# Optimization experiments

Hardware: AMD Instinct MI355X
Metric: run time of the kernel (lower is better)

## Reference

```python
import jax, jax.numpy as jnp
import numpy as np

A, B, S, AD, H, NH = 8, 32768, 128, 16, 64, 4
D = H // NH  # attend_dim = 16
MAX_ACTION = 1.0


def setup_inputs() -> dict:
    key = jax.random.key(0)
    ks = jax.random.split(key, 16)
    sc = 0.05
    return {
        'states': jax.random.normal(ks[0], (A, B, S), jnp.float32),
        'actions': jax.random.normal(ks[1], (A, B, AD), jnp.float32),
        'Ws': jax.random.normal(ks[2], (S, H), jnp.float32) * sc,
        'bs': jnp.zeros((H,), jnp.float32),
        'We': jax.random.normal(ks[3], (S + AD, H), jnp.float32) * sc,
        'be': jnp.zeros((H,), jnp.float32),
        'Wk': jax.random.normal(ks[4], (NH, H, D), jnp.float32) * sc,
        'Wsel': jax.random.normal(ks[5], (NH, H, D), jnp.float32) * sc,
        'Wv': jax.random.normal(ks[6], (NH, H, D), jnp.float32) * sc,
        'bv': jnp.zeros((NH, D), jnp.float32),
        'W1': jax.random.normal(ks[7], (2 * H, H), jnp.float32) * sc,
        'b1': jnp.zeros((H,), jnp.float32),
        'W2': jax.random.normal(ks[8], (H, 1), jnp.float32) * sc,
        'b2': jnp.zeros((1,), jnp.float32),
    }


def reference(states, actions, Ws, bs, We, be, Wk, Wsel, Wv, bv, W1, b1, W2, b2):
    # per-agent encoders (shared params, as in the torch module)
    s_enc = jax.nn.relu(jnp.einsum('abs,sh->abh', states, Ws) + bs)          # [A,B,H]
    sa = jnp.concatenate([states, actions / MAX_ACTION], axis=-1)            # [A,B,S+AD]
    sa_enc = jax.nn.relu(jnp.einsum('abi,ih->abh', sa, We) + be)             # [A,B,H]

    # per-head keys / values / selectors (n = head axis)
    keys = jnp.einsum('abh,nhd->nabd', sa_enc, Wk)                           # [NH,A,B,D]
    vals = jax.nn.relu(jnp.einsum('abh,nhd->nabd', sa_enc, Wv) + bv[:, None, None, :])
    sel = jnp.einsum('abh,nhd->nabd', s_enc, Wsel)                           # [NH,A,B,D]

    # exclude-self attention over agents == masked softmax over agent axis j
    logits = jnp.einsum('nibd,njbd->nibj', sel, keys) / jnp.sqrt(jnp.float32(D))
    self_mask = jnp.eye(A, dtype=bool)                                       # [A(i),A(j)]
    logits = jnp.where(self_mask[None, :, None, :], -1e9, logits)
    w = jax.nn.softmax(logits, axis=-1)                                      # [NH,A,B,A]
    other = jnp.einsum('nibj,njbd->nibd', w, vals)                           # [NH,A,B,D]
    other_cat = jnp.transpose(other, (1, 2, 0, 3)).reshape(A, B, NH * D)     # [A,B,H]

    critic_in = jnp.concatenate([sa_enc, other_cat], axis=-1)                # [A,B,2H]
    h = jax.nn.relu(jnp.einsum('abi,ih->abh', critic_in, W1) + b1)
    q = jnp.einsum('abh,ho->abo', h, W2) + b2                                # [A,B,1]
    return q
```

## Files before the change

kernel.cpp:

```cpp
#include <hip/hip_runtime.h>
#include <hip/hip_bf16.h>

#define A_N 8
#define B_N 32768
#define S_N 128
#define AD_N 16

typedef __attribute__((ext_vector_type(8))) short short8;
typedef __attribute__((ext_vector_type(4))) float floatx4;
typedef __attribute__((ext_vector_type(4))) int intx4;

#define MFMA16(a, b, c) __builtin_amdgcn_mfma_f32_16x16x32_bf16(a, b, c, 0, 0, 0)
#define SBAR() __builtin_amdgcn_sched_barrier(0)

__device__ __forceinline__ short f2bf(float f) {
    __hip_bfloat16 h = __float2bfloat16(f);
    return *reinterpret_cast<short*>(&h);
}
__device__ __forceinline__ int pk(float a, float b) {
    __hip_bfloat162 p = __float22bfloat162_rn(make_float2(a, b));
    return *reinterpret_cast<int*>(&p);
}
__device__ __forceinline__ short8 mk8(int a, int b, int c, int d) {
    intx4 v = {a, b, c, d};
    return *reinterpret_cast<short8*>(&v);
}
__device__ __forceinline__ void pk2(short8& r, int i, float a, float b) {
    __hip_bfloat162 p = __float22bfloat162_rn(make_float2(a, b));
    short2 s = *reinterpret_cast<short2*>(&p);
    r[i] = s.x; r[i + 1] = s.y;
}
__device__ __forceinline__ short8 cvt8(float4 x0, float4 x1) {
    short8 r;
    pk2(r, 0, x0.x, x0.y); pk2(r, 2, x0.z, x0.w);
    pk2(r, 4, x1.x, x1.y); pk2(r, 6, x1.z, x1.w);
    return r;
}

__device__ __forceinline__ int chperm(int p) {
    return 32 * (p >> 5) + 16 * ((p & 7) >> 2) + 4 * ((p >> 3) & 3) + (p & 3);
}

#define OFF_Ws   10752
#define OFF_Wk   21504
#define OFF_Wsel 26112
#define OFF_Wv   30720
#define OFF_W1   35328
#define W_TOTAL  44032

__global__ void prep_weights(const float* __restrict__ Ws, const float* __restrict__ bs,
                             const float* __restrict__ We, const float* __restrict__ be,
                             const float* __restrict__ Wk, const float* __restrict__ Wsel,
                             const float* __restrict__ Wv, const float* __restrict__ W1,
                             short* __restrict__ w) {
    int idx = blockIdx.x * 256 + threadIdx.x;
    if (idx >= W_TOTAL) return;
    float v = 0.f;
    if (idx < OFF_Ws) {
        int n = idx / 168, p = idx % 168;
        v = (p < 144) ? We[p * 64 + n] : (p == 144 ? be[n] : 0.f);
    } else if (idx < OFF_Wk) {
        int i = idx - OFF_Ws; int n = i / 168, p = i % 168;
        v = (p < 128) ? Ws[p * 64 + n] : (p == 144 ? bs[n] : 0.f);
    } else if (idx < OFF_Wsel) {
        int i = idx - OFF_Wk; int n = i / 72, p = i % 72;
        if (p < 64) v = Wk[(n >> 4) * 1024 + chperm(p) * 16 + (n & 15)];
    } else if (idx < OFF_Wv) {
        int i = idx - OFF_Wsel; int n = i / 72, p = i % 72;
        if (p < 64) v = Wsel[(n >> 4) * 1024 + chperm(p) * 16 + (n & 15)];
    } else if (idx < OFF_W1) {
        int i = idx - OFF_Wv; int n = i / 72, p = i % 72;
        if (p < 64) v = Wv[(n >> 4) * 1024 + chperm(p) * 16 + (n & 15)];
    } else {
        int i = idx - OFF_W1; int n = i / 136, p = i % 136;
        if (p < 128) v = W1[chperm(p) * 64 + n];
    }
    w[idx] = f2bf(v);
}

#define TILES 8

__global__ __launch_bounds__(512, 2)
void attention_critic_mfma(
    const float* __restrict__ states, const float* __restrict__ actions,
    const float* __restrict__ bv, const float* __restrict__ b1,
    const float* __restrict__ W2, const float* __restrict__ b2,
    const short* __restrict__ wts, float* __restrict__ out)
{
    __shared__ __align__(16) short smem[W_TOTAL];
    const short* lWe   = smem;
    const short* lWs   = smem + OFF_Ws;
    const short* lWk   = smem + OFF_Wk;
    const short* lWsel = smem + OFF_Wsel;
    const short* lWv   = smem + OFF_Wv;
    const short* lW1   = smem + OFF_W1;

    const int tid  = threadIdx.x;
    const int wv   = tid >> 6;
    const int lane = tid & 63;
    const int lq   = lane >> 4;
    const int ln   = lane & 15;

    for (int c = wv; c < 86; c += 8) {
        const unsigned int* g = reinterpret_cast<const unsigned int*>(wts + c * 512) + lane * 4;
        __builtin_amdgcn_global_load_lds(g, reinterpret_cast<unsigned int*>(smem + c * 512), 16, 0, 0);
    }

    float bv4[4], b14[4], w24[4];
    #pragma unroll
    for (int nt = 0; nt < 4; ++nt) {
        bv4[nt] = bv[nt * 16 + ln];
        b14[nt] = b1[nt * 16 + ln];
        w24[nt] = W2[nt * 16 + ln];
    }
    const float b2v = b2[0];

    const int bbase = blockIdx.x * (TILES * 16);
    const int aA  = ln & 7;
    const int blA = ln >> 3;
    const float* srow = states  + ((long)aA * B_N + bbase + wv * 2 + blA) * S_N;
    const float* arow = actions + ((long)aA * B_N + bbase + wv * 2 + blA) * AD_N;

    __syncthreads();

    const floatx4 z  = {0.f, 0.f, 0.f, 0.f};
    const short8  z8 = {0, 0, 0, 0, 0, 0, 0, 0};

    #pragma unroll 1
    for (int t = 0; t < TILES; ++t) {
        const int b0 = bbase + t * 16;

        short8 xf[5];
        #pragma unroll
        for (int s = 0; s < 4; ++s) {
            float4 f0 = *reinterpret_cast<const float4*>(srow + s * 32 + lq * 8);
            float4 f1 = *reinterpret_cast<const float4*>(srow + s * 32 + lq * 8 + 4);
            xf[s] = cvt8(f0, f1);
        }
        {
            short8 xt = z8;
            if (lq < 2) {
                float4 f0 = *reinterpret_cast<const float4*>(arow + lq * 8);
                float4 f1 = *reinterpret_cast<const float4*>(arow + lq * 8 + 4);
                xt = cvt8(f0, f1);
            } else if (lq == 2) {
                xt[0] = (short)0x3F80;
            }
            xf[4] = xt;
        }
        srow += 16 * S_N; arow += 16 * AD_N;

        short8 fE[2];
        {
            floatx4 accE[4] = {z, z, z, z};
            #pragma unroll
            for (int s = 0; s < 5; ++s) {
                const int kk = s * 32 + lq * 8;
                #pragma unroll
                for (int nt = 0; nt < 4; ++nt)
                    accE[nt] = MFMA16(*reinterpret_cast<const short8*>(lWe + (nt * 16 + ln) * 168 + kk), xf[s], accE[nt]);
            }
            int pE[4][2];
            #pragma unroll
            for (int nt = 0; nt < 4; ++nt) {
                pE[nt][0] = pk(fmaxf(accE[nt][0], 0.f), fmaxf(accE[nt][1], 0.f));
                pE[nt][1] = pk(fmaxf(accE[nt][2], 0.f), fmaxf(accE[nt][3], 0.f));
            }
            fE[0] = mk8(pE[0][0], pE[0][1], pE[1][0], pE[1][1]);
            fE[1] = mk8(pE[2][0], pE[2][1], pE[3][0], pE[3][1]);
        }
        SBAR();

        short8 fS[2];
        {
            floatx4 accS[4] = {z, z, z, z};
            #pragma unroll
            for (int s = 0; s < 5; ++s) {
                if (s == 4 && lq != 2) {
                }
                const int kk = s * 32 + lq * 8;
                #pragma unroll
                for (int nt = 0; nt < 4; ++nt)
                    accS[nt] = MFMA16(*reinterpret_cast<const short8*>(lWs + (nt * 16 + ln) * 168 + kk), xf[s], accS[nt]);
            }
            int pS[4][2];
            #pragma unroll
            for (int nt = 0; nt < 4; ++nt) {
                pS[nt][0] = pk(fmaxf(accS[nt][0], 0.f), fmaxf(accS[nt][1], 0.f));
                pS[nt][1] = pk(fmaxf(accS[nt][2], 0.f), fmaxf(accS[nt][3], 0.f));
            }
            fS[0] = mk8(pS[0][0], pS[0][1], pS[1][0], pS[1][1]);
            fS[1] = mk8(pS[2][0], pS[2][1], pS[3][0], pS[3][1]);
        }
        SBAR();

        int kp[4][2], sp[4][2];
        {
            floatx4 accK[4] = {z, z, z, z}, accSl[4] = {z, z, z, z};
            #pragma unroll
            for (int s = 0; s < 2; ++s) {
                const int kk = s * 32 + lq * 8;
                #pragma unroll
                for (int nt = 0; nt < 4; ++nt) {
                    const int rw = (nt * 16 + ln);
                    accK[nt]  = MFMA16(*reinterpret_cast<const short8*>(lWk   + rw * 72 + kk), fE[s], accK[nt]);
                    accSl[nt] = MFMA16(*reinterpret_cast<const short8*>(lWsel + rw * 72 + kk), fS[s], accSl[nt]);
                }
            }
            #pragma unroll
            for (int nt = 0; nt < 4; ++nt) {
                kp[nt][0] = pk(accK[nt][0],  accK[nt][1]);
                kp[nt][1] = pk(accK[nt][2],  accK[nt][3]);
                sp[nt][0] = pk(accSl[nt][0], accSl[nt][1]);
                sp[nt][1] = pk(accSl[nt][2], accSl[nt][3]);
            }
        }
        SBAR();

        int pV[4][2];
        {
            floatx4 accV[4] = {z, z, z, z};
            #pragma unroll
            for (int s = 0; s < 2; ++s) {
                const int kk = s * 32 + lq * 8;
                #pragma unroll
                for (int nt = 0; nt < 4; ++nt)
                    accV[nt] = MFMA16(fE[s], *reinterpret_cast<const short8*>(lWv + (nt * 16 + ln) * 72 + kk), accV[nt]);
            }
            #pragma unroll
            for (int nt = 0; nt < 4; ++nt) {
                pV[nt][0] = pk(fmaxf(accV[nt][0] + bv4[nt], 0.f), fmaxf(accV[nt][1] + bv4[nt], 0.f));
                pV[nt][1] = pk(fmaxf(accV[nt][2] + bv4[nt], 0.f), fmaxf(accV[nt][3] + bv4[nt], 0.f));
            }
        }
        SBAR();

        int pO[4][2];
        {
            const bool sameb = ((lq >> 1) == (ln >> 3));
            #pragma unroll
            for (int nt = 0; nt < 4; ++nt) {
                short8 fa = mk8(kp[nt][0], kp[nt][1], 0, 0);
                short8 fb = mk8(sp[nt][0], sp[nt][1], 0, 0);
                floatx4 L = MFMA16(fa, fb, z);
                float lg[4];
                #pragma unroll
                for (int i = 0; i < 4; ++i) {
                    const bool valid = sameb && (4 * lq + i != ln);
                    lg[i] = valid ? L[i] * 0.25f : -1e9f;
                }
                float m = fmaxf(fmaxf(lg[0], lg[1]), fmaxf(lg[2], lg[3]));
                m = fmaxf(m, __shfl_xor(m, 16, 64));
                m = fmaxf(m, __shfl_xor(m, 32, 64));
                float e0 = __expf(lg[0] - m), e1 = __expf(lg[1] - m);
                float e2 = __expf(lg[2] - m), e3 = __expf(lg[3] - m);
                float ss = e0 + e1 + e2 + e3;
                ss += __shfl_xor(ss, 16, 64);
                ss += __shfl_xor(ss, 32, 64);
                const float inv = 1.f / ss;
                short8 fp = mk8(pk(e0 * inv, e1 * inv), pk(e2 * inv, e3 * inv), 0, 0);
                short8 fv = mk8(pV[nt][0], pV[nt][1], 0, 0);
                floatx4 O = MFMA16(fv, fp, z);
                pO[nt][0] = pk(O[0], O[1]);
                pO[nt][1] = pk(O[2], O[3]);
            }
        }
        SBAR();

        {
            short8 fO[2] = { mk8(pO[0][0], pO[0][1], pO[1][0], pO[1][1]),
                             mk8(pO[2][0], pO[2][1], pO[3][0], pO[3][1]) };
            floatx4 accH[4] = {z, z, z, z};
            #pragma unroll
            for (int s = 0; s < 4; ++s) {
                const int kk = s * 32 + lq * 8;
                const short8 af = (s < 2) ? fE[s] : fO[s - 2];
                #pragma unroll
                for (int nt = 0; nt < 4; ++nt)
                    accH[nt] = MFMA16(af, *reinterpret_cast<const short8*>(lW1 + (nt * 16 + ln) * 136 + kk), accH[nt]);
            }
            float p0 = 0.f, p1 = 0.f, p2 = 0.f, p3 = 0.f;
            #pragma unroll
            for (int nt = 0; nt < 4; ++nt) {
                p0 += fmaxf(accH[nt][0] + b14[nt], 0.f) * w24[nt];
                p1 += fmaxf(accH[nt][1] + b14[nt], 0.f) * w24[nt];
                p2 += fmaxf(accH[nt][2] + b14[nt], 0.f) * w24[nt];
                p3 += fmaxf(accH[nt][3] + b14[nt], 0.f) * w24[nt];
            }
            #pragma unroll
            for (int mk = 1; mk < 16; mk <<= 1) {
                p0 += __shfl_xor(p0, mk, 64);
                p1 += __shfl_xor(p1, mk, 64);
                p2 += __shfl_xor(p2, mk, 64);
                p3 += __shfl_xor(p3, mk, 64);
            }
            if (ln == 0) {
                float pr[4] = {p0, p1, p2, p3};
                #pragma unroll
                for (int i = 0; i < 4; ++i) {
                    const int slot = lq * 4 + i;
                    out[(long)(slot & 7) * B_N + b0 + wv * 2 + (slot >> 3)] = pr[i] + b2v;
                }
            }
        }
        SBAR();
    }
}

extern "C" void kernel_launch(void* const* d_in, const int* in_sizes, int n_in,
                              void* d_out, int out_size, void* d_ws, size_t ws_size,
                              hipStream_t stream) {
    const float* states  = (const float*)d_in[0];
    const float* actions = (const float*)d_in[1];
    const float* Ws      = (const float*)d_in[2];
    const float* bs      = (const float*)d_in[3];
    const float* We      = (const float*)d_in[4];
    const float* be      = (const float*)d_in[5];
    const float* Wk      = (const float*)d_in[6];
    const float* Wsel    = (const float*)d_in[7];
    const float* Wv      = (const float*)d_in[8];
    const float* bv      = (const float*)d_in[9];
    const float* W1      = (const float*)d_in[10];
    const float* b1      = (const float*)d_in[11];
    const float* W2      = (const float*)d_in[12];
    const float* b2      = (const float*)d_in[13];
    short* wts = (short*)d_ws;
    float* out = (float*)d_out;

    prep_weights<<<(W_TOTAL + 255) / 256, 256, 0, stream>>>(Ws, bs, We, be, Wk, Wsel, Wv, W1, wts);
    attention_critic_mfma<<<B_N / (TILES * 16), 512, 0, stream>>>(
        states, actions, bv, b1, W2, b2, wts, out);
}
```

Baseline: 234.3 us.

## Repack LDS weights into MFMA fragment order and raise occupancy with smaller tiles

Reorders the bf16 weight blob so each lane's 8-element MFMA fragment sits contiguously in lane-major order, with no padding. This shrinks LDS from about 88KB to 78KB and gives simple constant-offset ds_read_b128 addresses. The s_enc bias moves out of the packed K=160 slot into a register add, which drops the fifth MFMA step for the Ws projection. TILES goes from 8 to 4, doubling the grid, and launch bounds ask for 4 blocks/CU, which may fail to fit LDS or may force register spilling.

```diff
diff --git a/kernel.cpp b/kernel.cpp
--- a/kernel.cpp
+++ b/kernel.cpp
@@ -41,59 +41,53 @@
     return 32 * (p >> 5) + 16 * ((p & 7) >> 2) + 4 * ((p >> 3) & 3) + (p & 3);
 }
 
-#define OFF_Ws   10752
-#define OFF_Wk   21504
-#define OFF_Wsel 26112
-#define OFF_Wv   30720
-#define OFF_W1   35328
-#define W_TOTAL  44032
-
-__global__ void prep_weights(const float* __restrict__ Ws, const float* __restrict__ bs,
-                             const float* __restrict__ We, const float* __restrict__ be,
+#define OFF_Ws   10240
+#define OFF_Wk   18432
+#define OFF_Wsel 22528
+#define OFF_Wv   26624
+#define OFF_W1   30720
+#define W_TOTAL  38912
+
+__global__ void prep_weights(const float* __restrict__ Ws, const float* __restrict__ We,
+                             const float* __restrict__ be,
                              const float* __restrict__ Wk, const float* __restrict__ Wsel,
                              const float* __restrict__ Wv, const float* __restrict__ W1,
                              short* __restrict__ w) {
     int idx = blockIdx.x * 256 + threadIdx.x;
     if (idx >= W_TOTAL) return;
     float v = 0.f;
-    if (idx < OFF_Ws) {
-        int n = idx / 168, p = idx % 168;
-        v = (p < 144) ? We[p * 64 + n] : (p == 144 ? be[n] : 0.f);
-    } else if (idx < OFF_Wk) {
-        int i = idx - OFF_Ws; int n = i / 168, p = i % 168;
-        v = (p < 128) ? Ws[p * 64 + n] : (p == 144 ? bs[n] : 0.f);
-    } else if (idx < OFF_Wsel) {
-        int i = idx - OFF_Wk; int n = i / 72, p = i % 72;
-        if (p < 64) v = Wk[(n >> 4) * 1024 + chperm(p) * 16 + (n & 15)];
-    } else if (idx < OFF_Wv) {
-        int i = idx - OFF_Wsel; int n = i / 72, p = i % 72;
-        if (p < 64) v = Wsel[(n >> 4) * 1024 + chperm(p) * 16 + (n & 15)];
-    } else if (idx < OFF_W1) {
-        int i = idx - OFF_Wv; int n = i / 72, p = i % 72;
-        if (p < 64) v = Wv[(n >> 4) * 1024 + chperm(p) * 16 + (n & 15)];
-    } else {
-        int i = idx - OFF_W1; int n = i / 136, p = i % 136;
-        if (p < 128) v = W1[chperm(p) * 64 + n];
-    }
+    int i, base;
+    if (idx < OFF_Ws)        { i = idx;            base = 0; }
+    else if (idx < OFF_Wk)   { i = idx - OFF_Ws;   base = 1; }
+    else if (idx < OFF_Wsel) { i = idx - OFF_Wk;   base = 2; }
+    else if (idx < OFF_Wv)   { i = idx - OFF_Wsel; base = 3; }
+    else if (idx < OFF_W1)   { i = idx - OFF_Wv;   base = 4; }
+    else                     { i = idx - OFF_W1;   base = 5; }
+    const int e   = i & 7;
+    const int f   = i >> 3;
+    const int ch  = f & 63;
+    const int slq = f >> 6;
+    const int p   = (slq >> 2) * 32 + (slq & 3) * 8 + e;
+    if (base == 0)      v = (p < 144) ? We[p * 64 + ch] : (p == 144 ? be[ch] : 0.f);
+    else if (base == 1) v = Ws[p * 64 + ch];
+    else if (base == 2) v = Wk[(ch >> 4) * 1024 + chperm(p) * 16 + (ch & 15)];
+    else if (base == 3) v = Wsel[(ch >> 4) * 1024 + chperm(p) * 16 + (ch & 15)];
+    else if (base == 4) v = Wv[(ch >> 4) * 1024 + chperm(p) * 16 + (ch & 15)];
+    else                v = W1[chperm(p) * 64 + ch];
     w[idx] = f2bf(v);
 }
 
-#define TILES 8
-
-__global__ __launch_bounds__(512, 2)
+#define TILES 4
+
+__global__ __launch_bounds__(512, 4)
 void attention_critic_mfma(
     const float* __restrict__ states, const float* __restrict__ actions,
-    const float* __restrict__ bv, const float* __restrict__ b1,
-    const float* __restrict__ W2, const float* __restrict__ b2,
+    const float* __restrict__ bs, const float* __restrict__ bv,
+    const float* __restrict__ b1, const float* __restrict__ W2,
+    const float* __restrict__ b2,
     const short* __restrict__ wts, float* __restrict__ out)
 {
     __shared__ __align__(16) short smem[W_TOTAL];
-    const short* lWe   = smem;
-    const short* lWs   = smem + OFF_Ws;
-    const short* lWk   = smem + OFF_Wk;
-    const short* lWsel = smem + OFF_Wsel;
-    const short* lWv   = smem + OFF_Wv;
-    const short* lW1   = smem + OFF_W1;
 
     const int tid  = threadIdx.x;
     const int wv   = tid >> 6;
@@ -101,14 +95,19 @@
     const int lq   = lane >> 4;
     const int ln   = lane & 15;
 
-    for (int c = wv; c < 86; c += 8) {
+    for (int c = wv; c < 76; c += 8) {
         const unsigned int* g = reinterpret_cast<const unsigned int*>(wts + c * 512) + lane * 4;
         __builtin_amdgcn_global_load_lds(g, reinterpret_cast<unsigned int*>(smem + c * 512), 16, 0, 0);
     }
 
-    float bv4[4], b14[4], w24[4];
+    const int lo = lq * 512 + ln * 8;
+    const short* lbA = smem + lo;
+    const short* lbB = smem + OFF_Wv + lo;
+
+    float bS4[4], bv4[4], b14[4], w24[4];
     #pragma unroll
     for (int nt = 0; nt < 4; ++nt) {
+        bS4[nt] = bs[nt * 16 + ln];
         bv4[nt] = bv[nt * 16 + ln];
         b14[nt] = b1[nt * 16 + ln];
         w24[nt] = W2[nt * 16 + ln];
@@ -123,8 +122,7 @@
 
     __syncthreads();
 
-    const floatx4 z  = {0.f, 0.f, 0.f, 0.f};
-    const short8  z8 = {0, 0, 0, 0, 0, 0, 0, 0};
+    const floatx4 z = {0.f, 0.f, 0.f, 0.f};
 
     #pragma unroll 1
     for (int t = 0; t < TILES; ++t) {
@@ -138,7 +136,7 @@
             xf[s] = cvt8(f0, f1);
         }
         {
-            short8 xt = z8;
+            short8 xt = {0, 0, 0, 0, 0, 0, 0, 0};
             if (lq < 2) {
                 float4 f0 = *reinterpret_cast<const float4*>(arow + lq * 8);
                 float4 f1 = *reinterpret_cast<const float4*>(arow + lq * 8 + 4);
@@ -154,12 +152,10 @@
         {
             floatx4 accE[4] = {z, z, z, z};
             #pragma unroll
-            for (int s = 0; s < 5; ++s) {
-                const int kk = s * 32 + lq * 8;
+            for (int s = 0; s < 5; ++s)
                 #pragma unroll
                 for (int nt = 0; nt < 4; ++nt)
-                    accE[nt] = MFMA16(*reinterpret_cast<const short8*>(lWe + (nt * 16 + ln) * 168 + kk), xf[s], accE[nt]);
-            }
+                    accE[nt] = MFMA16(*reinterpret_cast<const short8*>(lbA + s * 2048 + nt * 128), xf[s], accE[nt]);
             int pE[4][2];
             #pragma unroll
             for (int nt = 0; nt < 4; ++nt) {
@@ -175,19 +171,15 @@
         {
             floatx4 accS[4] = {z, z, z, z};
             #pragma unroll
-            for (int s = 0; s < 5; ++s) {
-                if (s == 4 && lq != 2) {
-                }
-                const int kk = s * 32 + lq * 8;
+            for (int s = 0; s < 4; ++s)
                 #pragma unroll
                 for (int nt = 0; nt < 4; ++nt)
-                    accS[nt] = MFMA16(*reinterpret_cast<const short8*>(lWs + (nt * 16 + ln) * 168 + kk), xf[s], accS[nt]);
-            }
+                    accS[nt] = MFMA16(*reinterpret_cast<const short8*>(lbA + OFF_Ws + s * 2048 + nt * 128), xf[s], accS[nt]);
             int pS[4][2];
             #pragma unroll
             for (int nt = 0; nt < 4; ++nt) {
-                pS[nt][0] = pk(fmaxf(accS[nt][0], 0.f), fmaxf(accS[nt][1], 0.f));
-                pS[nt][1] = pk(fmaxf(accS[nt][2], 0.f), fmaxf(accS[nt][3], 0.f));
+                pS[nt][0] = pk(fmaxf(accS[nt][0] + bS4[nt], 0.f), fmaxf(accS[nt][1] + bS4[nt], 0.f));
+                pS[nt][1] = pk(fmaxf(accS[nt][2] + bS4[nt], 0.f), fmaxf(accS[nt][3] + bS4[nt], 0.f));
             }
             fS[0] = mk8(pS[0][0], pS[0][1], pS[1][0], pS[1][1]);
             fS[1] = mk8(pS[2][0], pS[2][1], pS[3][0], pS[3][1]);
@@ -198,15 +190,12 @@
         {
             floatx4 accK[4] = {z, z, z, z}, accSl[4] = {z, z, z, z};
             #pragma unroll
-            for (int s = 0; s < 2; ++s) {
-                const int kk = s * 32 + lq * 8;
+            for (int s = 0; s < 2; ++s)
                 #pragma unroll
                 for (int nt = 0; nt < 4; ++nt) {
-                    const int rw = (nt * 16 + ln);
-                    accK[nt]  = MFMA16(*reinterpret_cast<const short8*>(lWk   + rw * 72 + kk), fE[s], accK[nt]);
-                    accSl[nt] = MFMA16(*reinterpret_cast<const short8*>(lWsel + rw * 72 + kk), fS[s], accSl[nt]);
+                    accK[nt]  = MFMA16(*reinterpret_cast<const short8*>(lbA + OFF_Wk   + s * 2048 + nt * 128), fE[s], accK[nt]);
+                    accSl[nt] = MFMA16(*reinterpret_cast<const short8*>(lbA + OFF_Wsel + s * 2048 + nt * 128), fS[s], accSl[nt]);
                 }
-            }
             #pragma unroll
             for (int nt = 0; nt < 4; ++nt) {
                 kp[nt][0] = pk(accK[nt][0],  accK[nt][1]);
@@ -221,12 +210,10 @@
         {
             floatx4 accV[4] = {z, z, z, z};
             #pragma unroll
-            for (int s = 0; s < 2; ++s) {
-                const int kk = s * 32 + lq * 8;
+            for (int s = 0; s < 2; ++s)
                 #pragma unroll
                 for (int nt = 0; nt < 4; ++nt)
-                    accV[nt] = MFMA16(fE[s], *reinterpret_cast<const short8*>(lWv + (nt * 16 + ln) * 72 + kk), accV[nt]);
-            }
+                    accV[nt] = MFMA16(fE[s], *reinterpret_cast<const short8*>(lbB + s * 2048 + nt * 128), accV[nt]);
             #pragma unroll
             for (int nt = 0; nt < 4; ++nt) {
                 pV[nt][0] = pk(fmaxf(accV[nt][0] + bv4[nt], 0.f), fmaxf(accV[nt][1] + bv4[nt], 0.f));
@@ -273,11 +260,10 @@
             floatx4 accH[4] = {z, z, z, z};
             #pragma unroll
             for (int s = 0; s < 4; ++s) {
-                const int kk = s * 32 + lq * 8;
                 const short8 af = (s < 2) ? fE[s] : fO[s - 2];
                 #pragma unroll
                 for (int nt = 0; nt < 4; ++nt)
-                    accH[nt] = MFMA16(af, *reinterpret_cast<const short8*>(lW1 + (nt * 16 + ln) * 136 + kk), accH[nt]);
+                    accH[nt] = MFMA16(af, *reinterpret_cast<const short8*>(lbB + 4096 + s * 2048 + nt * 128), accH[nt]);
             }
             float p0 = 0.f, p1 = 0.f, p2 = 0.f, p3 = 0.f;
             #pragma unroll
@@ -327,7 +313,7 @@
     short* wts = (short*)d_ws;
     float* out = (float*)d_out;
 
-    prep_weights<<<(W_TOTAL + 255) / 256, 256, 0, stream>>>(Ws, bs, We, be, Wk, Wsel, Wv, W1, wts);
+    prep_weights<<<(W_TOTAL + 255) / 256, 256, 0, stream>>>(Ws, We, be, Wk, Wsel, Wv, W1, wts);
     attention_critic_mfma<<<B_N / (TILES * 16), 512, 0, stream>>>(
-        states, actions, bv, b1, W2, b2, wts, out);
-}
+        states, actions, bs, bv, b1, W2, b2, wts, out);
+}
```

Result: no change. 234.3 us (-0.0%).
